# Performance work log

Measured on AMD Instinct MI355X. Metric: run time of the kernel, lower is better.

## Reference

```python
import jax, jax.numpy as jnp
import numpy as np

SQRT_DK = jnp.sqrt(jnp.float32(128.0))
BN_EPS = 1e-5


def setup_inputs() -> dict:
    key = jax.random.key(0)
    ks = jax.random.split(key, 12)
    B, C, F, Fp, K, O, DK = 4, 64, 20000, 10000, 16, 128, 128
    fea = jax.random.normal(ks[0], (B, C, F), dtype=jnp.float32)
    ring_n = jax.random.randint(ks[1], (B, Fp, K), 0, F, dtype=jnp.int64)
    pool_idx = jnp.sort(jax.random.randint(ks[2], (Fp,), 0, F, dtype=jnp.int64))
    pos_embed = jnp.zeros((1, 1, 1), dtype=jnp.float32)
    s = 1.0 / np.sqrt(C)
    Wk = jax.random.uniform(ks[3], (DK, C), jnp.float32, -s, s)
    bk = jax.random.uniform(ks[4], (DK,), jnp.float32, -s, s)
    Wq = jax.random.uniform(ks[5], (DK, C), jnp.float32, -s, s)
    bq = jax.random.uniform(ks[6], (DK,), jnp.float32, -s, s)
    Wc = jax.random.uniform(ks[7], (O, C), jnp.float32, -s, s)
    bc = jax.random.uniform(ks[8], (O,), jnp.float32, -s, s)
    gamma = jnp.ones((O,), jnp.float32)
    beta = jnp.zeros((O,), jnp.float32)
    return {"fea": fea, "ring_n": ring_n, "pool_idx": pool_idx, "pos_embed": pos_embed,
            "Wk": Wk, "bk": bk, "Wq": Wq, "bq": bq, "Wc": Wc, "bc": bc,
            "gamma": gamma, "beta": beta}


def _gather_neighbors(fea, ring_n):
    # fea: [B,C,F], ring_n: [B,Fp,K] -> [B,C,Fp,K]
    return jax.vmap(lambda f, r: f[:, r])(fea, ring_n)


def reference(fea, ring_n, pool_idx, pos_embed, Wk, bk, Wq, bq, Wc, bc, gamma, beta):
    # neighbor gather along face dim
    neighbor_fea = _gather_neighbors(fea, ring_n)            # [B,C,Fp,K]
    self_fea = fea[:, :, pool_idx][..., None]                # [B,C,Fp,1]
    cat = jnp.concatenate([self_fea, neighbor_fea], axis=3)  # [B,C,Fp,K+1]
    # per-face key (self only) and per-neighbor query (Linear4D over channel dim)
    keyv = jnp.einsum('bcfk,oc->bofk', self_fea, Wk) + bk[None, :, None, None]  # [B,128,Fp,1]
    query = jnp.einsum('bcfk,oc->bofk', cat, Wq) + bq[None, :, None, None]       # [B,128,Fp,K+1]
    att = jnp.sum(keyv * query, axis=1, keepdims=True) / SQRT_DK                 # [B,1,Fp,K+1]
    att = jax.nn.softmax(att, axis=3)
    agg = jnp.sum(cat * att, axis=3)                                             # [B,C,Fp]
    # concat_mlp: 1x1 conv + BatchNorm1d (training-mode batch stats) + ReLU
    y = jnp.einsum('bcf,oc->bof', agg, Wc) + bc[None, :, None]                   # [B,O,Fp]
    mean = jnp.mean(y, axis=(0, 2), keepdims=True)
    var = jnp.var(y, axis=(0, 2), keepdims=True)
    y = (y - mean) * jax.lax.rsqrt(var + BN_EPS)
    y = y * gamma[None, :, None] + beta[None, :, None]
    return jax.nn.relu(y)
```

## Files before the change

kernel.cpp:

```cpp
#include <hip/hip_runtime.h>

#define F_ALL 20000
#define FP    10000
#define BB    4
#define KK    16
#define OO    128
#define NFACE 40000
#define NBLK  625

#define WS_FEAT 0
#define WS_AGG  (BB*F_ALL*64)
#define WS_GP   (WS_AGG + NFACE*64)
#define WS_SAP  (WS_GP + NBLK*4096)
#define WS_MT   (WS_SAP + NBLK*64)
#define WS_V0   (WS_MT + 4096)
#define WS_G    (WS_V0 + 64)
#define WS_SUMA (WS_G + 4096)
#define WS_SC   (WS_SUMA + 64)
#define WS_SH   (WS_SC + 128)

template<int CTRL>
__device__ __forceinline__ float dpp_add(float x) {
    return x + __int_as_float(__builtin_amdgcn_update_dpp(0, __float_as_int(x), CTRL, 0xF, 0xF, true));
}
__device__ __forceinline__ float sum16(float x) {
    x = dpp_add<0x121>(x);
    x = dpp_add<0x122>(x);
    x = dpp_add<0x124>(x);
    x = dpp_add<0x128>(x);
    return x;
}

__global__ __launch_bounds__(256) void k_pre(const float* __restrict__ fea,
                                             const float* __restrict__ Wk,
                                             const float* __restrict__ bk,
                                             const float* __restrict__ Wq,
                                             float* __restrict__ ws) {
    __shared__ float tile[64][65];
    int tid = threadIdx.x;
    if (blockIdx.x < 1252) {
        int bb = blockIdx.x / 313;
        int tb = blockIdx.x % 313;
        int fbase = tb * 64;
        int x  = tid & 63;
        int y0 = tid >> 6;
        int f = fbase + x;
        float* feaT = ws + WS_FEAT;
        if (f < F_ALL) {
#pragma unroll
            for (int i = 0; i < 16; i++) {
                int c = y0 + i * 4;
                tile[c][x] = fea[((long)bb * 64 + c) * F_ALL + f];
            }
        }
        __syncthreads();
#pragma unroll
        for (int i = 0; i < 16; i++) {
            int fr = y0 + i * 4;
            int ff = fbase + fr;
            if (ff < F_ALL)
                feaT[((long)bb * F_ALL + ff) * 64 + x] = tile[x][fr];
        }
    } else {
        int idx = (blockIdx.x - 1252) * 256 + tid;
        int j = idx >> 6, i = idx & 63;
        float acc = 0.f;
#pragma unroll 8
        for (int o = 0; o < 128; o++) acc += Wq[o * 64 + i] * Wk[o * 64 + j];
        ws[WS_MT + idx] = acc;
        if (blockIdx.x == 1252 && tid < 64) {
            float a = 0.f;
            for (int o = 0; o < 128; o++) a += Wq[o * 64 + tid] * bk[o];
            ws[WS_V0 + tid] = a;
            ws[WS_SUMA + tid] = 0.f;
        }
    }
}

__global__ __launch_bounds__(256) void k_attn(const int* __restrict__ ring,
                                              const int* __restrict__ pool,
                                              float* __restrict__ ws) {
    __shared__ __align__(16) float lds[12608];
    float* At = lds;
    float* Sf = lds + 4096;
    float* U  = lds + 8256;
    int tid = threadIdx.x;
    int fbase = blockIdx.x * 64;
    const float* feaT = ws + WS_FEAT;
    const float scale = 0.08838834764831845f;

    for (int i = tid; i < 4096; i += 256) At[i] = ws[WS_MT + i];
    {
        int r = tid >> 2;
        int face = fbase + r;
        int b = face / FP;
        int p = pool[face - b * FP];
        const float* src = feaT + ((long)(b * F_ALL + p)) * 64;
        int off = (tid & 3) * 4;
#pragma unroll
        for (int it = 0; it < 4; it++, off += 16) {
            float4 v = *(const float4*)(src + off);
            Sf[r * 65 + off + 0] = v.x;
            Sf[r * 65 + off + 1] = v.y;
            Sf[r * 65 + off + 2] = v.z;
            Sf[r * 65 + off + 3] = v.w;
        }
    }
    __syncthreads();

    int ti = tid & 15, tj = tid >> 4;
    {
        int f0 = ti * 4, o0 = tj * 4;
        float4 v0 = *(const float4*)&ws[WS_V0 + o0];
        float acc[4][4];
#pragma unroll
        for (int a = 0; a < 4; a++) {
            acc[a][0] = v0.x; acc[a][1] = v0.y; acc[a][2] = v0.z; acc[a][3] = v0.w;
        }
        for (int j = 0; j < 64; j++) {
            float4 wv = *(const float4*)&At[j * 64 + o0];
#pragma unroll
            for (int a = 0; a < 4; a++) {
                float av = Sf[(f0 + a) * 65 + j];
                acc[a][0] += av * wv.x;
                acc[a][1] += av * wv.y;
                acc[a][2] += av * wv.z;
                acc[a][3] += av * wv.w;
            }
        }
#pragma unroll
        for (int a = 0; a < 4; a++)
            *(float4*)&U[(f0 + a) * 68 + o0] =
                make_float4(acc[a][0], acc[a][1], acc[a][2], acc[a][3]);
    }
    __syncthreads();

    float* Ag = At;
    int lane = tid & 63;
    int il = lane & 15, c4 = il * 4;
    for (int it = 0; it < 4; it++) {
        int fl = (tid >> 4) + it * 16;
        int face = fbase + fl;
        int b = face / FP;
        const float* fb = feaT + ((long)b * F_ALL) * 64 + c4;

        float4 sf = make_float4(Sf[fl * 65 + c4], Sf[fl * 65 + c4 + 1],
                                Sf[fl * 65 + c4 + 2], Sf[fl * 65 + c4 + 3]);
        float4 u = *(const float4*)&U[fl * 68 + c4];

        int rv = ring[face * KK + il];
        float4 nv[KK];
#pragma unroll
        for (int k = 0; k < KK; k++) {
            int rk = __shfl(rv, (lane & 48) | k, 64);
            nv[k] = *(const float4*)(fb + (long)rk * 64);
        }

        float l[KK + 1];
        l[0] = sum16(u.x * sf.x + u.y * sf.y + u.z * sf.z + u.w * sf.w) * scale;
#pragma unroll
        for (int k = 0; k < KK; k++)
            l[k + 1] = sum16(u.x * nv[k].x + u.y * nv[k].y + u.z * nv[k].z + u.w * nv[k].w) * scale;

        float m = l[0];
#pragma unroll
        for (int k = 1; k <= KK; k++) m = fmaxf(m, l[k]);
        float den = 0.f;
#pragma unroll
        for (int k = 0; k <= KK; k++) { l[k] = __expf(l[k] - m); den += l[k]; }
        float inv = 1.0f / den;

        float4 a;
        a.x = l[0] * sf.x; a.y = l[0] * sf.y; a.z = l[0] * sf.z; a.w = l[0] * sf.w;
#pragma unroll
        for (int k = 0; k < KK; k++) {
            a.x += l[k + 1] * nv[k].x;
            a.y += l[k + 1] * nv[k].y;
            a.z += l[k + 1] * nv[k].z;
            a.w += l[k + 1] * nv[k].w;
        }
        a.x *= inv; a.y *= inv; a.z *= inv; a.w *= inv;
        *(float4*)&Ag[fl * 64 + c4] = a;
        *(float4*)&ws[WS_AGG + (long)face * 64 + c4] = a;
    }
    __syncthreads();

    float acc[4][4];
#pragma unroll
    for (int a = 0; a < 4; a++)
#pragma unroll
        for (int b = 0; b < 4; b++) acc[a][b] = 0.f;
    float gacc[4] = {0.f, 0.f, 0.f, 0.f};
#pragma unroll 4
    for (int f = 0; f < 64; f++) {
        float4 av = *(const float4*)&Ag[f * 64 + ti * 4];
        float4 bv = *(const float4*)&Ag[f * 64 + tj * 4];
        float avv[4] = {av.x, av.y, av.z, av.w};
        float bvv[4] = {bv.x, bv.y, bv.z, bv.w};
#pragma unroll
        for (int a = 0; a < 4; a++) {
#pragma unroll
            for (int b = 0; b < 4; b++) acc[a][b] += avv[a] * bvv[b];
            gacc[a] += avv[a];
        }
    }
    float* gp = ws + WS_GP;
#pragma unroll
    for (int a = 0; a < 4; a++)
        *(float4*)&gp[(long)blockIdx.x * 4096 + (ti * 4 + a) * 64 + tj * 4] =
            make_float4(acc[a][0], acc[a][1], acc[a][2], acc[a][3]);
    if (tj == 0)
        *(float4*)&ws[WS_SAP + blockIdx.x * 64 + ti * 4] =
            make_float4(gacc[0], gacc[1], gacc[2], gacc[3]);
}

__global__ __launch_bounds__(256) void k_gsum(float* __restrict__ ws) {
    __shared__ float red[256];
    int t = threadIdx.x;
    if (blockIdx.x < 256) {
        const float* gp = ws + WS_GP;
        int e16 = blockIdx.x * 16;
        int e = t & 15, c = t >> 4;
        int p0 = c * 40;
        int p1 = p0 + 40; if (p1 > NBLK) p1 = NBLK;
        float s0 = 0.f, s1 = 0.f, s2 = 0.f, s3 = 0.f;
        int p = p0;
        for (; p + 4 <= p1; p += 4) {
            s0 += gp[(long)(p + 0) * 4096 + e16 + e];
            s1 += gp[(long)(p + 1) * 4096 + e16 + e];
            s2 += gp[(long)(p + 2) * 4096 + e16 + e];
            s3 += gp[(long)(p + 3) * 4096 + e16 + e];
        }
        for (; p < p1; p++) s0 += gp[(long)p * 4096 + e16 + e];
        red[t] = (s0 + s1) + (s2 + s3);
        __syncthreads();
        if (t < 16) {
            float s = 0.f;
#pragma unroll
            for (int cc = 0; cc < 16; cc++) s += red[cc * 16 + t];
            ws[WS_G + e16 + t] = s;
        }
    } else {
        const float* sap = ws + WS_SAP;
        int bq = blockIdx.x - 256;
        int e = t & 63, c = t >> 6;
        int pidx = bq * 4 + c;
        int p0 = pidx * 40;
        int p1 = p0 + 40; if (p1 > NBLK) p1 = NBLK;
        float s0 = 0.f, s1 = 0.f, s2 = 0.f, s3 = 0.f;
        int p = p0;
        for (; p + 4 <= p1; p += 4) {
            s0 += sap[(p + 0) * 64 + e];
            s1 += sap[(p + 1) * 64 + e];
            s2 += sap[(p + 2) * 64 + e];
            s3 += sap[(p + 3) * 64 + e];
        }
        for (; p < p1; p++) s0 += sap[p * 64 + e];
        red[t] = (s0 + s1) + (s2 + s3);
        __syncthreads();
        if (t < 64) {
            float tot = red[t] + red[t + 64] + red[t + 128] + red[t + 192];
            atomicAdd(&ws[WS_SUMA + t], tot);
        }
    }
}

__global__ __launch_bounds__(256) void k_stats(const float* __restrict__ Wc,
                                               const float* __restrict__ bc,
                                               const float* __restrict__ gamma,
                                               const float* __restrict__ beta,
                                               float* __restrict__ ws) {
    __shared__ float Gs[4096];
    __shared__ float gs[64];
    __shared__ float qs[256];
    int tid = threadIdx.x;
    for (int i = tid; i < 4096; i += 256) Gs[i] = ws[WS_G + i];
    if (tid < 64) gs[tid] = ws[WS_SUMA + tid];
    __syncthreads();

    int o = tid & 127, h = tid >> 7;
    float w[64];
#pragma unroll
    for (int q = 0; q < 16; q++) {
        float4 t = *(const float4*)&Wc[o * 64 + q * 4];
        w[q * 4 + 0] = t.x; w[q * 4 + 1] = t.y; w[q * 4 + 2] = t.z; w[q * 4 + 3] = t.w;
    }
    float qp = 0.f;
    for (int i = h * 32; i < h * 32 + 32; i++) {
        float t = 0.f;
#pragma unroll
        for (int j = 0; j < 64; j++) t += Gs[i * 64 + j] * w[j];
        qp += Wc[o * 64 + i] * t;
    }
    qs[tid] = qp;
    __syncthreads();
    if (h == 0) {
        const float invN = 1.0f / (float)NFACE;
        float qform = qs[o] + qs[o + 128];
        float md = 0.f;
#pragma unroll
        for (int j = 0; j < 64; j++) md += gs[j] * w[j];
        float bco = bc[o];
        float mean = md * invN + bco;
        float ey2  = (qform + 2.f * bco * md) * invN + bco * bco;
        float var  = ey2 - mean * mean;
        float sc   = gamma[o] * rsqrtf(var + 1e-5f);
        ws[WS_SC + o] = sc;
        ws[WS_SH + o] = beta[o] + (bco - mean) * sc;
    }
}

__global__ __launch_bounds__(256) void k_out(const float* __restrict__ Wc,
                                             const float* __restrict__ ws,
                                             float* __restrict__ out) {
    __shared__ __align__(16) float WcT[64 * 132];
    __shared__ __align__(16) float AgT[64 * 68];
    const float* agg = ws + WS_AGG;
    int tid = threadIdx.x;
    int fbase = blockIdx.x * 64;
    for (int i = tid; i < 128 * 64; i += 256) {
        int o = i >> 6, j = i & 63;
        WcT[j * 132 + o] = Wc[i];
    }
    for (int i = tid; i < 64 * 64; i += 256) {
        int f = i >> 6, j = i & 63;
        AgT[j * 68 + f] = agg[((long)(fbase + f)) * 64 + j];
    }
    __syncthreads();

    int tx = tid & 15, ty = tid >> 4;
    float acc[8][4];
#pragma unroll
    for (int a = 0; a < 8; a++)
#pragma unroll
        for (int b = 0; b < 4; b++) acc[a][b] = 0.f;

    for (int j = 0; j < 64; j++) {
        float4 w0 = *(const float4*)&WcT[j * 132 + ty * 8];
        float4 w1 = *(const float4*)&WcT[j * 132 + ty * 8 + 4];
        float4 a0 = *(const float4*)&AgT[j * 68 + tx * 4];
        float wv[8] = {w0.x, w0.y, w0.z, w0.w, w1.x, w1.y, w1.z, w1.w};
        float av[4] = {a0.x, a0.y, a0.z, a0.w};
#pragma unroll
        for (int oi = 0; oi < 8; oi++)
#pragma unroll
            for (int fi = 0; fi < 4; fi++) acc[oi][fi] += wv[oi] * av[fi];
    }

    int fg0 = fbase + tx * 4;
    int b   = fg0 / FP;
    int fp0 = fg0 - b * FP;
#pragma unroll
    for (int oi = 0; oi < 8; oi++) {
        int o = ty * 8 + oi;
        float sc = ws[WS_SC + o];
        float sh = ws[WS_SH + o];
        float4 v;
        v.x = fmaxf(acc[oi][0] * sc + sh, 0.f);
        v.y = fmaxf(acc[oi][1] * sc + sh, 0.f);
        v.z = fmaxf(acc[oi][2] * sc + sh, 0.f);
        v.w = fmaxf(acc[oi][3] * sc + sh, 0.f);
        *(float4*)&out[((long)(b * OO + o)) * FP + fp0] = v;
    }
}

extern "C" void kernel_launch(void* const* d_in, const int* in_sizes, int n_in,
                              void* d_out, int out_size, void* d_ws, size_t ws_size,
                              hipStream_t stream) {
    const float* fea  = (const float*)d_in[0];
    const int*   ring = (const int*)d_in[1];
    const int*   pool = (const int*)d_in[2];
    const float* Wk = (const float*)d_in[4];
    const float* bk = (const float*)d_in[5];
    const float* Wq = (const float*)d_in[6];
    const float* Wc = (const float*)d_in[8];
    const float* bc = (const float*)d_in[9];
    const float* gamma = (const float*)d_in[10];
    const float* beta  = (const float*)d_in[11];

    float* out = (float*)d_out;
    float* ws  = (float*)d_ws;

    k_pre  <<<1268, 256, 0, stream>>>(fea, Wk, bk, Wq, ws);
    k_attn <<<NBLK, 256, 0, stream>>>(ring, pool, ws);
    k_gsum <<<260,  256, 0, stream>>>(ws);
    k_stats<<<1,    256, 0, stream>>>(Wc, bc, gamma, beta, ws);
    k_out  <<<NBLK, 256, 0, stream>>>(Wc, ws, out);
}
```

Measured before the change: 173.8 us.

## Fuse all stages into one persistent cooperative kernel with grid syncs

Merges the five separate kernels into a single persistent cooperative kernel that loops over tiles and separates phases with grid-wide syncs. It falls back to four phased launches if the cooperative launch fails. Stats are now computed redundantly per block and kept in LDS instead of in a separate single-block kernel and global scratch. The aim is to remove launch gaps and the serial single-block stats launch, at the cost of grid.sync overhead, reduced occupancy (launch bounds of 2 blocks per CU, grid capped at 625), and a host occupancy query on every call.

Measured after the change: 300.8 us. 73.1% more time.

```diff
diff --git a/kernel.cpp b/kernel.cpp
--- a/kernel.cpp
+++ b/kernel.cpp
@@ -1,4 +1,7 @@
 #include <hip/hip_runtime.h>
+#include <hip/hip_cooperative_groups.h>
+
+namespace cg = cooperative_groups;
 
 #define F_ALL 20000
 #define FP    10000
@@ -6,18 +9,22 @@
 #define KK    16
 #define OO    128
 #define NFACE 40000
-#define NBLK  625
+#define NTILE 625
 
 #define WS_FEAT 0
 #define WS_AGG  (BB*F_ALL*64)
 #define WS_GP   (WS_AGG + NFACE*64)
-#define WS_SAP  (WS_GP + NBLK*4096)
-#define WS_MT   (WS_SAP + NBLK*64)
+#define WS_SAP  (WS_GP + NTILE*4096)
+#define WS_MT   (WS_SAP + NTILE*64)
 #define WS_V0   (WS_MT + 4096)
 #define WS_G    (WS_V0 + 64)
 #define WS_SUMA (WS_G + 4096)
-#define WS_SC   (WS_SUMA + 64)
-#define WS_SH   (WS_SC + 128)
+
+#define L_R1   4352
+#define L_GS   8448
+#define L_QS   8512
+#define L_SC   12800
+#define L_SH   12928
 
 template<int CTRL>
 __device__ __forceinline__ float dpp_add(float x) {
@@ -31,336 +38,363 @@
     return x;
 }
 
-__global__ __launch_bounds__(256) void k_pre(const float* __restrict__ fea,
-                                             const float* __restrict__ Wk,
-                                             const float* __restrict__ bk,
-                                             const float* __restrict__ Wq,
-                                             float* __restrict__ ws) {
-    __shared__ float tile[64][65];
-    int tid = threadIdx.x;
-    if (blockIdx.x < 1252) {
-        int bb = blockIdx.x / 313;
-        int tb = blockIdx.x % 313;
-        int fbase = tb * 64;
-        int x  = tid & 63;
-        int y0 = tid >> 6;
-        int f = fbase + x;
+__global__ __launch_bounds__(256, 2) void k_fused(const float* __restrict__ fea,
+                                                  const int* __restrict__ ring,
+                                                  const int* __restrict__ pool,
+                                                  const float* __restrict__ Wk,
+                                                  const float* __restrict__ bk,
+                                                  const float* __restrict__ Wq,
+                                                  const float* __restrict__ Wc,
+                                                  const float* __restrict__ bc,
+                                                  const float* __restrict__ gamma,
+                                                  const float* __restrict__ beta,
+                                                  float* __restrict__ ws,
+                                                  float* __restrict__ out,
+                                                  int phase) {
+    __shared__ __align__(16) float lds[13056];
+    cg::grid_group grid = cg::this_grid();
+    const int tid  = threadIdx.x;
+    const int bid  = blockIdx.x;
+    const int GRID = gridDim.x;
+    const bool coop = (phase < 0);
+    const float scale = 0.08838834764831845f;
+
+    if (coop || phase == 0) {
+        float* tile = lds;
         float* feaT = ws + WS_FEAT;
-        if (f < F_ALL) {
+        for (int tb = bid; tb < 1252; tb += GRID) {
+            __syncthreads();
+            int bb = tb / 313;
+            int fbase = (tb % 313) * 64;
+            int x  = tid & 63;
+            int y0 = tid >> 6;
+            int f = fbase + x;
+            if (f < F_ALL) {
+#pragma unroll
+                for (int i = 0; i < 16; i++) {
+                    int c = y0 + i * 4;
+                    tile[c * 65 + x] = fea[((long)bb * 64 + c) * F_ALL + f];
+                }
+            }
+            __syncthreads();
 #pragma unroll
             for (int i = 0; i < 16; i++) {
-                int c = y0 + i * 4;
-                tile[c][x] = fea[((long)bb * 64 + c) * F_ALL + f];
-            }
-        }
-        __syncthreads();
-#pragma unroll
-        for (int i = 0; i < 16; i++) {
-            int fr = y0 + i * 4;
-            int ff = fbase + fr;
-            if (ff < F_ALL)
-                feaT[((long)bb * F_ALL + ff) * 64 + x] = tile[x][fr];
-        }
-    } else {
-        int idx = (blockIdx.x - 1252) * 256 + tid;
-        int j = idx >> 6, i = idx & 63;
-        float acc = 0.f;
+                int fr = y0 + i * 4;
+                int ff = fbase + fr;
+                if (ff < F_ALL)
+                    feaT[((long)bb * F_ALL + ff) * 64 + x] = tile[x * 65 + fr];
+            }
+        }
+        if (bid < 16) {
+            int idx = bid * 256 + tid;
+            int j = idx >> 6, i = idx & 63;
+            float acc = 0.f;
 #pragma unroll 8
-        for (int o = 0; o < 128; o++) acc += Wq[o * 64 + i] * Wk[o * 64 + j];
-        ws[WS_MT + idx] = acc;
-        if (blockIdx.x == 1252 && tid < 64) {
+            for (int o = 0; o < 128; o++) acc += Wq[o * 64 + i] * Wk[o * 64 + j];
+            ws[WS_MT + idx] = acc;
+        } else if (bid == 16 && tid < 64) {
             float a = 0.f;
             for (int o = 0; o < 128; o++) a += Wq[o * 64 + tid] * bk[o];
             ws[WS_V0 + tid] = a;
             ws[WS_SUMA + tid] = 0.f;
         }
     }
-}
-
-__global__ __launch_bounds__(256) void k_attn(const int* __restrict__ ring,
-                                              const int* __restrict__ pool,
-                                              float* __restrict__ ws) {
-    __shared__ __align__(16) float lds[12608];
-    float* At = lds;
-    float* Sf = lds + 4096;
-    float* U  = lds + 8256;
-    int tid = threadIdx.x;
-    int fbase = blockIdx.x * 64;
-    const float* feaT = ws + WS_FEAT;
-    const float scale = 0.08838834764831845f;
-
-    for (int i = tid; i < 4096; i += 256) At[i] = ws[WS_MT + i];
-    {
-        int r = tid >> 2;
-        int face = fbase + r;
-        int b = face / FP;
-        int p = pool[face - b * FP];
-        const float* src = feaT + ((long)(b * F_ALL + p)) * 64;
-        int off = (tid & 3) * 4;
-#pragma unroll
-        for (int it = 0; it < 4; it++, off += 16) {
-            float4 v = *(const float4*)(src + off);
-            Sf[r * 65 + off + 0] = v.x;
-            Sf[r * 65 + off + 1] = v.y;
-            Sf[r * 65 + off + 2] = v.z;
-            Sf[r * 65 + off + 3] = v.w;
-        }
-    }
-    __syncthreads();
-
-    int ti = tid & 15, tj = tid >> 4;
-    {
-        int f0 = ti * 4, o0 = tj * 4;
-        float4 v0 = *(const float4*)&ws[WS_V0 + o0];
-        float acc[4][4];
-#pragma unroll
-        for (int a = 0; a < 4; a++) {
-            acc[a][0] = v0.x; acc[a][1] = v0.y; acc[a][2] = v0.z; acc[a][3] = v0.w;
-        }
-        for (int j = 0; j < 64; j++) {
-            float4 wv = *(const float4*)&At[j * 64 + o0];
-#pragma unroll
-            for (int a = 0; a < 4; a++) {
-                float av = Sf[(f0 + a) * 65 + j];
-                acc[a][0] += av * wv.x;
-                acc[a][1] += av * wv.y;
-                acc[a][2] += av * wv.z;
-                acc[a][3] += av * wv.w;
-            }
-        }
-#pragma unroll
-        for (int a = 0; a < 4; a++)
-            *(float4*)&U[(f0 + a) * 68 + o0] =
-                make_float4(acc[a][0], acc[a][1], acc[a][2], acc[a][3]);
-    }
-    __syncthreads();
-
-    float* Ag = At;
-    int lane = tid & 63;
-    int il = lane & 15, c4 = il * 4;
-    for (int it = 0; it < 4; it++) {
-        int fl = (tid >> 4) + it * 16;
-        int face = fbase + fl;
-        int b = face / FP;
-        const float* fb = feaT + ((long)b * F_ALL) * 64 + c4;
-
-        float4 sf = make_float4(Sf[fl * 65 + c4], Sf[fl * 65 + c4 + 1],
-                                Sf[fl * 65 + c4 + 2], Sf[fl * 65 + c4 + 3]);
-        float4 u = *(const float4*)&U[fl * 68 + c4];
-
-        int rv = ring[face * KK + il];
-        float4 nv[KK];
-#pragma unroll
-        for (int k = 0; k < KK; k++) {
-            int rk = __shfl(rv, (lane & 48) | k, 64);
-            nv[k] = *(const float4*)(fb + (long)rk * 64);
-        }
-
-        float l[KK + 1];
-        l[0] = sum16(u.x * sf.x + u.y * sf.y + u.z * sf.z + u.w * sf.w) * scale;
-#pragma unroll
-        for (int k = 0; k < KK; k++)
-            l[k + 1] = sum16(u.x * nv[k].x + u.y * nv[k].y + u.z * nv[k].z + u.w * nv[k].w) * scale;
-
-        float m = l[0];
-#pragma unroll
-        for (int k = 1; k <= KK; k++) m = fmaxf(m, l[k]);
-        float den = 0.f;
-#pragma unroll
-        for (int k = 0; k <= KK; k++) { l[k] = __expf(l[k] - m); den += l[k]; }
-        float inv = 1.0f / den;
-
-        float4 a;
-        a.x = l[0] * sf.x; a.y = l[0] * sf.y; a.z = l[0] * sf.z; a.w = l[0] * sf.w;
-#pragma unroll
-        for (int k = 0; k < KK; k++) {
-            a.x += l[k + 1] * nv[k].x;
-            a.y += l[k + 1] * nv[k].y;
-            a.z += l[k + 1] * nv[k].z;
-            a.w += l[k + 1] * nv[k].w;
-        }
-        a.x *= inv; a.y *= inv; a.z *= inv; a.w *= inv;
-        *(float4*)&Ag[fl * 64 + c4] = a;
-        *(float4*)&ws[WS_AGG + (long)face * 64 + c4] = a;
-    }
-    __syncthreads();
-
-    float acc[4][4];
-#pragma unroll
-    for (int a = 0; a < 4; a++)
-#pragma unroll
-        for (int b = 0; b < 4; b++) acc[a][b] = 0.f;
-    float gacc[4] = {0.f, 0.f, 0.f, 0.f};
+    if (coop) grid.sync();
+
+    if (coop || phase == 1) {
+        float* Sf = lds;
+        float* U  = lds + L_R1;
+        float* At = lds + 8704;
+        const float* feaT = ws + WS_FEAT;
+        int ti = tid & 15, tj = tid >> 4;
+        int lane = tid & 63;
+        int il = lane & 15, c4 = il * 4;
+
+        for (int i = tid; i < 4096; i += 256) At[i] = ws[WS_MT + i];
+
+        for (int tile = bid; tile < NTILE; tile += GRID) {
+            int fbase = tile * 64;
+            __syncthreads();
+
+            {
+                int r = tid >> 2;
+                int face = fbase + r;
+                int b = face / FP;
+                int p = pool[face - b * FP];
+                const float* src = feaT + ((long)(b * F_ALL + p)) * 64;
+                int off = (tid & 3) * 4;
+#pragma unroll
+                for (int it = 0; it < 4; it++, off += 16) {
+                    float4 v = *(const float4*)(src + off);
+                    Sf[r * 65 + off + 0] = v.x;
+                    Sf[r * 65 + off + 1] = v.y;
+                    Sf[r * 65 + off + 2] = v.z;
+                    Sf[r * 65 + off + 3] = v.w;
+                }
+            }
+            __syncthreads();
+
+            {
+                int f0 = ti * 4, o0 = tj * 4;
+                float4 v0 = *(const float4*)&ws[WS_V0 + o0];
+                float acc[4][4];
+#pragma unroll
+                for (int a = 0; a < 4; a++) {
+                    acc[a][0] = v0.x; acc[a][1] = v0.y; acc[a][2] = v0.z; acc[a][3] = v0.w;
+                }
+                for (int j = 0; j < 64; j++) {
+                    float4 wv = *(const float4*)&At[j * 64 + o0];
+#pragma unroll
+                    for (int a = 0; a < 4; a++) {
+                        float av = Sf[(f0 + a) * 65 + j];
+                        acc[a][0] += av * wv.x;
+                        acc[a][1] += av * wv.y;
+                        acc[a][2] += av * wv.z;
+                        acc[a][3] += av * wv.w;
+                    }
+                }
+#pragma unroll
+                for (int a = 0; a < 4; a++)
+                    *(float4*)&U[(f0 + a) * 68 + o0] =
+                        make_float4(acc[a][0], acc[a][1], acc[a][2], acc[a][3]);
+            }
+            __syncthreads();
+
+            float4 a_res[4];
+            for (int it = 0; it < 4; it++) {
+                int fl = (tid >> 4) + it * 16;
+                int face = fbase + fl;
+                int b = face / FP;
+                const float* fb = feaT + ((long)b * F_ALL) * 64 + c4;
+
+                float4 sf = make_float4(Sf[fl * 65 + c4], Sf[fl * 65 + c4 + 1],
+                                        Sf[fl * 65 + c4 + 2], Sf[fl * 65 + c4 + 3]);
+                float4 u = *(const float4*)&U[fl * 68 + c4];
+
+                int rv = ring[face * KK + il];
+                float4 nv[KK];
+#pragma unroll
+                for (int k = 0; k < KK; k++) {
+                    int rk = __shfl(rv, (lane & 48) | k, 64);
+                    nv[k] = *(const float4*)(fb + (long)rk * 64);
+                }
+
+                float l[KK + 1];
+                l[0] = sum16(u.x * sf.x + u.y * sf.y + u.z * sf.z + u.w * sf.w) * scale;
+#pragma unroll
+                for (int k = 0; k < KK; k++)
+                    l[k + 1] = sum16(u.x * nv[k].x + u.y * nv[k].y + u.z * nv[k].z + u.w * nv[k].w) * scale;
+
+                float m = l[0];
+#pragma unroll
+                for (int k = 1; k <= KK; k++) m = fmaxf(m, l[k]);
+                float den = 0.f;
+#pragma unroll
+                for (int k = 0; k <= KK; k++) { l[k] = __expf(l[k] - m); den += l[k]; }
+                float inv = 1.0f / den;
+
+                float4 a;
+                a.x = l[0] * sf.x; a.y = l[0] * sf.y; a.z = l[0] * sf.z; a.w = l[0] * sf.w;
+#pragma unroll
+                for (int k = 0; k < KK; k++) {
+                    a.x += l[k + 1] * nv[k].x;
+                    a.y += l[k + 1] * nv[k].y;
+                    a.z += l[k + 1] * nv[k].z;
+                    a.w += l[k + 1] * nv[k].w;
+                }
+                a.x *= inv; a.y *= inv; a.z *= inv; a.w *= inv;
+                a_res[it] = a;
+                *(float4*)&ws[WS_AGG + (long)face * 64 + c4] = a;
+            }
+            __syncthreads();
+            float* Ag = lds;
+#pragma unroll
+            for (int it = 0; it < 4; it++) {
+                int fl = (tid >> 4) + it * 16;
+                *(float4*)&Ag[fl * 64 + c4] = a_res[it];
+            }
+            __syncthreads();
+
+            float acc[4][4];
+#pragma unroll
+            for (int a = 0; a < 4; a++)
+#pragma unroll
+                for (int b = 0; b < 4; b++) acc[a][b] = 0.f;
+            float gacc[4] = {0.f, 0.f, 0.f, 0.f};
 #pragma unroll 4
-    for (int f = 0; f < 64; f++) {
-        float4 av = *(const float4*)&Ag[f * 64 + ti * 4];
-        float4 bv = *(const float4*)&Ag[f * 64 + tj * 4];
-        float avv[4] = {av.x, av.y, av.z, av.w};
-        float bvv[4] = {bv.x, bv.y, bv.z, bv.w};
-#pragma unroll
-        for (int a = 0; a < 4; a++) {
-#pragma unroll
-            for (int b = 0; b < 4; b++) acc[a][b] += avv[a] * bvv[b];
-            gacc[a] += avv[a];
-        }
-    }
-    float* gp = ws + WS_GP;
-#pragma unroll
-    for (int a = 0; a < 4; a++)
-        *(float4*)&gp[(long)blockIdx.x * 4096 + (ti * 4 + a) * 64 + tj * 4] =
-            make_float4(acc[a][0], acc[a][1], acc[a][2], acc[a][3]);
-    if (tj == 0)
-        *(float4*)&ws[WS_SAP + blockIdx.x * 64 + ti * 4] =
-            make_float4(gacc[0], gacc[1], gacc[2], gacc[3]);
-}
-
-__global__ __launch_bounds__(256) void k_gsum(float* __restrict__ ws) {
-    __shared__ float red[256];
-    int t = threadIdx.x;
-    if (blockIdx.x < 256) {
-        const float* gp = ws + WS_GP;
-        int e16 = blockIdx.x * 16;
-        int e = t & 15, c = t >> 4;
-        int p0 = c * 40;
-        int p1 = p0 + 40; if (p1 > NBLK) p1 = NBLK;
-        float s0 = 0.f, s1 = 0.f, s2 = 0.f, s3 = 0.f;
-        int p = p0;
-        for (; p + 4 <= p1; p += 4) {
-            s0 += gp[(long)(p + 0) * 4096 + e16 + e];
-            s1 += gp[(long)(p + 1) * 4096 + e16 + e];
-            s2 += gp[(long)(p + 2) * 4096 + e16 + e];
-            s3 += gp[(long)(p + 3) * 4096 + e16 + e];
-        }
-        for (; p < p1; p++) s0 += gp[(long)p * 4096 + e16 + e];
-        red[t] = (s0 + s1) + (s2 + s3);
-        __syncthreads();
-        if (t < 16) {
-            float s = 0.f;
-#pragma unroll
-            for (int cc = 0; cc < 16; cc++) s += red[cc * 16 + t];
-            ws[WS_G + e16 + t] = s;
-        }
-    } else {
-        const float* sap = ws + WS_SAP;
-        int bq = blockIdx.x - 256;
-        int e = t & 63, c = t >> 6;
-        int pidx = bq * 4 + c;
-        int p0 = pidx * 40;
-        int p1 = p0 + 40; if (p1 > NBLK) p1 = NBLK;
-        float s0 = 0.f, s1 = 0.f, s2 = 0.f, s3 = 0.f;
-        int p = p0;
-        for (; p + 4 <= p1; p += 4) {
-            s0 += sap[(p + 0) * 64 + e];
-            s1 += sap[(p + 1) * 64 + e];
-            s2 += sap[(p + 2) * 64 + e];
-            s3 += sap[(p + 3) * 64 + e];
-        }
-        for (; p < p1; p++) s0 += sap[p * 64 + e];
-        red[t] = (s0 + s1) + (s2 + s3);
-        __syncthreads();
-        if (t < 64) {
-            float tot = red[t] + red[t + 64] + red[t + 128] + red[t + 192];
-            atomicAdd(&ws[WS_SUMA + t], tot);
-        }
-    }
-}
-
-__global__ __launch_bounds__(256) void k_stats(const float* __restrict__ Wc,
-                                               const float* __restrict__ bc,
-                                               const float* __restrict__ gamma,
-                                               const float* __restrict__ beta,
-                                               float* __restrict__ ws) {
-    __shared__ float Gs[4096];
-    __shared__ float gs[64];
-    __shared__ float qs[256];
-    int tid = threadIdx.x;
-    for (int i = tid; i < 4096; i += 256) Gs[i] = ws[WS_G + i];
-    if (tid < 64) gs[tid] = ws[WS_SUMA + tid];
-    __syncthreads();
-
-    int o = tid & 127, h = tid >> 7;
-    float w[64];
-#pragma unroll
-    for (int q = 0; q < 16; q++) {
-        float4 t = *(const float4*)&Wc[o * 64 + q * 4];
-        w[q * 4 + 0] = t.x; w[q * 4 + 1] = t.y; w[q * 4 + 2] = t.z; w[q * 4 + 3] = t.w;
-    }
-    float qp = 0.f;
-    for (int i = h * 32; i < h * 32 + 32; i++) {
-        float t = 0.f;
-#pragma unroll
-        for (int j = 0; j < 64; j++) t += Gs[i * 64 + j] * w[j];
-        qp += Wc[o * 64 + i] * t;
-    }
-    qs[tid] = qp;
-    __syncthreads();
-    if (h == 0) {
-        const float invN = 1.0f / (float)NFACE;
-        float qform = qs[o] + qs[o + 128];
-        float md = 0.f;
-#pragma unroll
-        for (int j = 0; j < 64; j++) md += gs[j] * w[j];
-        float bco = bc[o];
-        float mean = md * invN + bco;
-        float ey2  = (qform + 2.f * bco * md) * invN + bco * bco;
-        float var  = ey2 - mean * mean;
-        float sc   = gamma[o] * rsqrtf(var + 1e-5f);
-        ws[WS_SC + o] = sc;
-        ws[WS_SH + o] = beta[o] + (bco - mean) * sc;
-    }
-}
-
-__global__ __launch_bounds__(256) void k_out(const float* __restrict__ Wc,
-                                             const float* __restrict__ ws,
-                                             float* __restrict__ out) {
-    __shared__ __align__(16) float WcT[64 * 132];
-    __shared__ __align__(16) float AgT[64 * 68];
-    const float* agg = ws + WS_AGG;
-    int tid = threadIdx.x;
-    int fbase = blockIdx.x * 64;
-    for (int i = tid; i < 128 * 64; i += 256) {
-        int o = i >> 6, j = i & 63;
-        WcT[j * 132 + o] = Wc[i];
-    }
-    for (int i = tid; i < 64 * 64; i += 256) {
-        int f = i >> 6, j = i & 63;
-        AgT[j * 68 + f] = agg[((long)(fbase + f)) * 64 + j];
-    }
-    __syncthreads();
-
-    int tx = tid & 15, ty = tid >> 4;
-    float acc[8][4];
-#pragma unroll
-    for (int a = 0; a < 8; a++)
-#pragma unroll
-        for (int b = 0; b < 4; b++) acc[a][b] = 0.f;
-
-    for (int j = 0; j < 64; j++) {
-        float4 w0 = *(const float4*)&WcT[j * 132 + ty * 8];
-        float4 w1 = *(const float4*)&WcT[j * 132 + ty * 8 + 4];
-        float4 a0 = *(const float4*)&AgT[j * 68 + tx * 4];
-        float wv[8] = {w0.x, w0.y, w0.z, w0.w, w1.x, w1.y, w1.z, w1.w};
-        float av[4] = {a0.x, a0.y, a0.z, a0.w};
-#pragma unroll
-        for (int oi = 0; oi < 8; oi++)
-#pragma unroll
-            for (int fi = 0; fi < 4; fi++) acc[oi][fi] += wv[oi] * av[fi];
-    }
-
-    int fg0 = fbase + tx * 4;
-    int b   = fg0 / FP;
-    int fp0 = fg0 - b * FP;
-#pragma unroll
-    for (int oi = 0; oi < 8; oi++) {
-        int o = ty * 8 + oi;
-        float sc = ws[WS_SC + o];
-        float sh = ws[WS_SH + o];
-        float4 v;
-        v.x = fmaxf(acc[oi][0] * sc + sh, 0.f);
-        v.y = fmaxf(acc[oi][1] * sc + sh, 0.f);
-        v.z = fmaxf(acc[oi][2] * sc + sh, 0.f);
-        v.w = fmaxf(acc[oi][3] * sc + sh, 0.f);
-        *(float4*)&out[((long)(b * OO + o)) * FP + fp0] = v;
+            for (int f = 0; f < 64; f++) {
+                float4 av = *(const float4*)&Ag[f * 64 + ti * 4];
+                float4 bv = *(const float4*)&Ag[f * 64 + tj * 4];
+                float avv[4] = {av.x, av.y, av.z, av.w};
+                float bvv[4] = {bv.x, bv.y, bv.z, bv.w};
+#pragma unroll
+                for (int a = 0; a < 4; a++) {
+#pragma unroll
+                    for (int b = 0; b < 4; b++) acc[a][b] += avv[a] * bvv[b];
+                    gacc[a] += avv[a];
+                }
+            }
+            float* gp = ws + WS_GP;
+#pragma unroll
+            for (int a = 0; a < 4; a++)
+                *(float4*)&gp[(long)tile * 4096 + (ti * 4 + a) * 64 + tj * 4] =
+                    make_float4(acc[a][0], acc[a][1], acc[a][2], acc[a][3]);
+            if (tj == 0)
+                *(float4*)&ws[WS_SAP + tile * 64 + ti * 4] =
+                    make_float4(gacc[0], gacc[1], gacc[2], gacc[3]);
+        }
+    }
+    if (coop) grid.sync();
+
+    if (coop || phase == 2) {
+        float* red = lds;
+        for (int v = bid; v < 260; v += GRID) {
+            __syncthreads();
+            if (v < 256) {
+                const float* gp = ws + WS_GP;
+                int e16 = v * 16;
+                int e = tid & 15, c = tid >> 4;
+                int p0 = c * 40;
+                int p1 = p0 + 40; if (p1 > NTILE) p1 = NTILE;
+                float s0 = 0.f, s1 = 0.f, s2 = 0.f, s3 = 0.f;
+                int p = p0;
+                for (; p + 4 <= p1; p += 4) {
+                    s0 += gp[(long)(p + 0) * 4096 + e16 + e];
+                    s1 += gp[(long)(p + 1) * 4096 + e16 + e];
+                    s2 += gp[(long)(p + 2) * 4096 + e16 + e];
+                    s3 += gp[(long)(p + 3) * 4096 + e16 + e];
+                }
+                for (; p < p1; p++) s0 += gp[(long)p * 4096 + e16 + e];
+                red[tid] = (s0 + s1) + (s2 + s3);
+                __syncthreads();
+                if (tid < 16) {
+                    float s = 0.f;
+#pragma unroll
+                    for (int cc = 0; cc < 16; cc++) s += red[cc * 16 + tid];
+                    ws[WS_G + e16 + tid] = s;
+                }
+            } else {
+                const float* sap = ws + WS_SAP;
+                int bq = v - 256;
+                int e = tid & 63, c = tid >> 6;
+                int pidx = bq * 4 + c;
+                int p0 = pidx * 40;
+                int p1 = p0 + 40; if (p1 > NTILE) p1 = NTILE;
+                float s0 = 0.f, s1 = 0.f, s2 = 0.f, s3 = 0.f;
+                int p = p0;
+                for (; p + 4 <= p1; p += 4) {
+                    s0 += sap[(p + 0) * 64 + e];
+                    s1 += sap[(p + 1) * 64 + e];
+                    s2 += sap[(p + 2) * 64 + e];
+                    s3 += sap[(p + 3) * 64 + e];
+                }
+                for (; p < p1; p++) s0 += sap[p * 64 + e];
+                red[tid] = (s0 + s1) + (s2 + s3);
+                __syncthreads();
+                if (tid < 64) {
+                    float tot = red[tid] + red[tid + 64] + red[tid + 128] + red[tid + 192];
+                    atomicAdd(&ws[WS_SUMA + tid], tot);
+                }
+            }
+        }
+    }
+    if (coop) grid.sync();
+
+    if (coop || phase == 3) {
+        {
+            float* Gs = lds + L_R1;
+            float* gs = lds + L_GS;
+            float* qs = lds + L_QS;
+            __syncthreads();
+            for (int i = tid; i < 4096; i += 256) Gs[i] = ws[WS_G + i];
+            if (tid < 64) gs[tid] = ws[WS_SUMA + tid];
+            __syncthreads();
+
+            int o = tid & 127, h = tid >> 7;
+            float w[64];
+#pragma unroll
+            for (int q = 0; q < 16; q++) {
+                float4 t = *(const float4*)&Wc[o * 64 + q * 4];
+                w[q * 4 + 0] = t.x; w[q * 4 + 1] = t.y; w[q * 4 + 2] = t.z; w[q * 4 + 3] = t.w;
+            }
+            float qp = 0.f;
+            for (int i = h * 32; i < h * 32 + 32; i++) {
+                float t = 0.f;
+#pragma unroll
+                for (int j = 0; j < 64; j++) t += Gs[i * 64 + j] * w[j];
+                qp += Wc[o * 64 + i] * t;
+            }
+            qs[tid] = qp;
+            __syncthreads();
+            if (h == 0) {
+                const float invN = 1.0f / (float)NFACE;
+                float qform = qs[o] + qs[o + 128];
+                float md = 0.f;
+#pragma unroll
+                for (int j = 0; j < 64; j++) md += gs[j] * w[j];
+                float bco = bc[o];
+                float mean = md * invN + bco;
+                float ey2  = (qform + 2.f * bco * md) * invN + bco * bco;
+                float var  = ey2 - mean * mean;
+                float sc   = gamma[o] * rsqrtf(var + 1e-5f);
+                lds[L_SC + o] = sc;
+                lds[L_SH + o] = beta[o] + (bco - mean) * sc;
+            }
+            __syncthreads();
+        }
+        {
+            float* AgT = lds;
+            float* WcT = lds + L_R1;
+            const float* agg = ws + WS_AGG;
+            for (int i = tid; i < 128 * 64; i += 256) {
+                int o = i >> 6, j = i & 63;
+                WcT[j * 132 + o] = Wc[i];
+            }
+            int tx = tid & 15, ty = tid >> 4;
+            for (int tile = bid; tile < NTILE; tile += GRID) {
+                int fbase = tile * 64;
+                __syncthreads();
+                for (int i = tid; i < 64 * 64; i += 256) {
+                    int f = i >> 6, j = i & 63;
+                    AgT[j * 68 + f] = agg[((long)(fbase + f)) * 64 + j];
+                }
+                __syncthreads();
+
+                float acc[8][4];
+#pragma unroll
+                for (int a = 0; a < 8; a++)
+#pragma unroll
+                    for (int b = 0; b < 4; b++) acc[a][b] = 0.f;
+
+                for (int j = 0; j < 64; j++) {
+                    float4 w0 = *(const float4*)&WcT[j * 132 + ty * 8];
+                    float4 w1 = *(const float4*)&WcT[j * 132 + ty * 8 + 4];
+                    float4 a0 = *(const float4*)&AgT[j * 68 + tx * 4];
+                    float wv[8] = {w0.x, w0.y, w0.z, w0.w, w1.x, w1.y, w1.z, w1.w};
+                    float av[4] = {a0.x, a0.y, a0.z, a0.w};
+#pragma unroll
+                    for (int oi = 0; oi < 8; oi++)
+#pragma unroll
+                        for (int fi = 0; fi < 4; fi++) acc[oi][fi] += wv[oi] * av[fi];
+                }
+
+                int fg0 = fbase + tx * 4;
+                int b   = fg0 / FP;
+                int fp0 = fg0 - b * FP;
+#pragma unroll
+                for (int oi = 0; oi < 8; oi++) {
+                    int o = ty * 8 + oi;
+                    float sc = lds[L_SC + o];
+                    float sh = lds[L_SH + o];
+                    float4 v;
+                    v.x = fmaxf(acc[oi][0] * sc + sh, 0.f);
+                    v.y = fmaxf(acc[oi][1] * sc + sh, 0.f);
+                    v.z = fmaxf(acc[oi][2] * sc + sh, 0.f);
+                    v.w = fmaxf(acc[oi][3] * sc + sh, 0.f);
+                    *(float4*)&out[((long)(b * OO + o)) * FP + fp0] = v;
+                }
+            }
+        }
     }
 }
 
@@ -381,9 +415,22 @@
     float* out = (float*)d_out;
     float* ws  = (float*)d_ws;
 
-    k_pre  <<<1268, 256, 0, stream>>>(fea, Wk, bk, Wq, ws);
-    k_attn <<<NBLK, 256, 0, stream>>>(ring, pool, ws);
-    k_gsum <<<260,  256, 0, stream>>>(ws);
-    k_stats<<<1,    256, 0, stream>>>(Wc, bc, gamma, beta, ws);
-    k_out  <<<NBLK, 256, 0, stream>>>(Wc, ws, out);
+    int maxb = 0;
+    hipError_t qe = hipOccupancyMaxActiveBlocksPerMultiprocessor(&maxb, (const void*)k_fused, 256, 0);
+    int grid = (qe == hipSuccess && maxb > 0) ? maxb * 256 : 0;
+    if (grid > NTILE) grid = NTILE;
+
+    hipError_t le = hipErrorUnknown;
+    if (grid >= 64) {
+        int phase = -1;
+        void* kargs[] = {(void*)&fea, (void*)&ring, (void*)&pool, (void*)&Wk, (void*)&bk,
+                         (void*)&Wq, (void*)&Wc, (void*)&bc, (void*)&gamma, (void*)&beta,
+                         (void*)&ws, (void*)&out, (void*)&phase};
+        le = hipLaunchCooperativeKernel((const void*)k_fused, dim3(grid), dim3(256), kargs, 0, stream);
+    }
+    if (le != hipSuccess) {
+        for (int ph = 0; ph < 4; ph++)
+            k_fused<<<512, 256, 0, stream>>>(fea, ring, pool, Wk, bk, Wq, Wc, bc,
+                                             gamma, beta, ws, out, ph);
+    }
 }
```

## Split Gram accumulation into separate kernel and shrink attention blocks to 32 faces

Applied to the files above, without the earlier changes.

The attention kernel now handles 32 faces per block instead of 64. It computes each face's query-key projection inline per lane group rather than as a separate block GEMM stage with extra barriers, and drops the U and aggregated-tile LDS buffers. This cuts shared memory per block to raise occupancy for the latency-bound neighbor gather. The Gram and column-sum accumulation moves to a new k_gram kernel that rereads the aggregated features from global memory over 320 faces per block. That yields fewer partials to reduce, at the cost of an extra launch and an extra pass over the aggregate buffer.

Result: slower. 181.6 us (+4.5%).

```diff
diff --git a/kernel.cpp b/kernel.cpp
--- a/kernel.cpp
+++ b/kernel.cpp
@@ -6,13 +6,13 @@
 #define KK    16
 #define OO    128
 #define NFACE 40000
-#define NBLK  625
+#define NGRAMB 125
 
 #define WS_FEAT 0
 #define WS_AGG  (BB*F_ALL*64)
 #define WS_GP   (WS_AGG + NFACE*64)
-#define WS_SAP  (WS_GP + NBLK*4096)
-#define WS_MT   (WS_SAP + NBLK*64)
+#define WS_SAP  (WS_GP + NGRAMB*4096)
+#define WS_MT   (WS_SAP + NGRAMB*64)
 #define WS_V0   (WS_MT + 4096)
 #define WS_G    (WS_V0 + 64)
 #define WS_SUMA (WS_G + 4096)
@@ -80,65 +80,33 @@
 __global__ __launch_bounds__(256) void k_attn(const int* __restrict__ ring,
                                               const int* __restrict__ pool,
                                               float* __restrict__ ws) {
-    __shared__ __align__(16) float lds[12608];
-    float* At = lds;
-    float* Sf = lds + 4096;
-    float* U  = lds + 8256;
-    int tid = threadIdx.x;
-    int fbase = blockIdx.x * 64;
+    __shared__ __align__(16) float MTl[4096];
+    __shared__ float Sf[32 * 65];
+    int tid = threadIdx.x;
+    int fbase = blockIdx.x * 32;
     const float* feaT = ws + WS_FEAT;
     const float scale = 0.08838834764831845f;
 
-    for (int i = tid; i < 4096; i += 256) At[i] = ws[WS_MT + i];
+    for (int i = tid; i < 4096; i += 256) MTl[i] = ws[WS_MT + i];
     {
-        int r = tid >> 2;
+        int r = tid >> 3;
         int face = fbase + r;
         int b = face / FP;
         int p = pool[face - b * FP];
-        const float* src = feaT + ((long)(b * F_ALL + p)) * 64;
-        int off = (tid & 3) * 4;
-#pragma unroll
-        for (int it = 0; it < 4; it++, off += 16) {
-            float4 v = *(const float4*)(src + off);
-            Sf[r * 65 + off + 0] = v.x;
-            Sf[r * 65 + off + 1] = v.y;
-            Sf[r * 65 + off + 2] = v.z;
-            Sf[r * 65 + off + 3] = v.w;
-        }
+        const float* src = feaT + ((long)(b * F_ALL + p)) * 64 + (tid & 7) * 8;
+        float4 v0 = *(const float4*)src;
+        float4 v1 = *(const float4*)(src + 4);
+        float* dst = &Sf[r * 65 + (tid & 7) * 8];
+        dst[0] = v0.x; dst[1] = v0.y; dst[2] = v0.z; dst[3] = v0.w;
+        dst[4] = v1.x; dst[5] = v1.y; dst[6] = v1.z; dst[7] = v1.w;
     }
     __syncthreads();
 
-    int ti = tid & 15, tj = tid >> 4;
-    {
-        int f0 = ti * 4, o0 = tj * 4;
-        float4 v0 = *(const float4*)&ws[WS_V0 + o0];
-        float acc[4][4];
-#pragma unroll
-        for (int a = 0; a < 4; a++) {
-            acc[a][0] = v0.x; acc[a][1] = v0.y; acc[a][2] = v0.z; acc[a][3] = v0.w;
-        }
-        for (int j = 0; j < 64; j++) {
-            float4 wv = *(const float4*)&At[j * 64 + o0];
-#pragma unroll
-            for (int a = 0; a < 4; a++) {
-                float av = Sf[(f0 + a) * 65 + j];
-                acc[a][0] += av * wv.x;
-                acc[a][1] += av * wv.y;
-                acc[a][2] += av * wv.z;
-                acc[a][3] += av * wv.w;
-            }
-        }
-#pragma unroll
-        for (int a = 0; a < 4; a++)
-            *(float4*)&U[(f0 + a) * 68 + o0] =
-                make_float4(acc[a][0], acc[a][1], acc[a][2], acc[a][3]);
-    }
-    __syncthreads();
-
-    float* Ag = At;
     int lane = tid & 63;
     int il = lane & 15, c4 = il * 4;
-    for (int it = 0; it < 4; it++) {
+    float4 uv0 = *(const float4*)&ws[WS_V0 + c4];
+
+    for (int it = 0; it < 2; it++) {
         int fl = (tid >> 4) + it * 16;
         int face = fbase + fl;
         int b = face / FP;
@@ -146,7 +114,6 @@
 
         float4 sf = make_float4(Sf[fl * 65 + c4], Sf[fl * 65 + c4 + 1],
                                 Sf[fl * 65 + c4 + 2], Sf[fl * 65 + c4 + 3]);
-        float4 u = *(const float4*)&U[fl * 68 + c4];
 
         int rv = ring[face * KK + il];
         float4 nv[KK];
@@ -154,6 +121,17 @@
         for (int k = 0; k < KK; k++) {
             int rk = __shfl(rv, (lane & 48) | k, 64);
             nv[k] = *(const float4*)(fb + (long)rk * 64);
+        }
+
+        float4 u = uv0;
+#pragma unroll 8
+        for (int j = 0; j < 64; j++) {
+            float aj = Sf[fl * 65 + j];
+            float4 m4 = *(const float4*)&MTl[j * 64 + c4];
+            u.x += m4.x * aj;
+            u.y += m4.y * aj;
+            u.z += m4.z * aj;
+            u.w += m4.w * aj;
         }
 
         float l[KK + 1];
@@ -180,28 +158,41 @@
             a.w += l[k + 1] * nv[k].w;
         }
         a.x *= inv; a.y *= inv; a.z *= inv; a.w *= inv;
-        *(float4*)&Ag[fl * 64 + c4] = a;
         *(float4*)&ws[WS_AGG + (long)face * 64 + c4] = a;
     }
-    __syncthreads();
-
+}
+
+__global__ __launch_bounds__(256) void k_gram(float* __restrict__ ws) {
+    __shared__ float lbuf[4096];
+    const float* agg = ws + WS_AGG;
+    int tid = threadIdx.x;
+    int ti = tid & 15, tj = tid >> 4;
     float acc[4][4];
 #pragma unroll
     for (int a = 0; a < 4; a++)
 #pragma unroll
         for (int b = 0; b < 4; b++) acc[a][b] = 0.f;
     float gacc[4] = {0.f, 0.f, 0.f, 0.f};
+
+    for (int c = 0; c < 5; c++) {
+        int fbase = blockIdx.x * 320 + c * 64;
+        const float4* src = (const float4*)(agg + (long)fbase * 64);
+        float4* dst = (float4*)lbuf;
+        __syncthreads();
+        for (int i = tid; i < 1024; i += 256) dst[i] = src[i];
+        __syncthreads();
 #pragma unroll 4
-    for (int f = 0; f < 64; f++) {
-        float4 av = *(const float4*)&Ag[f * 64 + ti * 4];
-        float4 bv = *(const float4*)&Ag[f * 64 + tj * 4];
-        float avv[4] = {av.x, av.y, av.z, av.w};
-        float bvv[4] = {bv.x, bv.y, bv.z, bv.w};
-#pragma unroll
-        for (int a = 0; a < 4; a++) {
-#pragma unroll
-            for (int b = 0; b < 4; b++) acc[a][b] += avv[a] * bvv[b];
-            gacc[a] += avv[a];
+        for (int f = 0; f < 64; f++) {
+            float4 av = *(const float4*)&lbuf[f * 64 + ti * 4];
+            float4 bv = *(const float4*)&lbuf[f * 64 + tj * 4];
+            float avv[4] = {av.x, av.y, av.z, av.w};
+            float bvv[4] = {bv.x, bv.y, bv.z, bv.w};
+#pragma unroll
+            for (int a = 0; a < 4; a++) {
+#pragma unroll
+                for (int b = 0; b < 4; b++) acc[a][b] += avv[a] * bvv[b];
+                gacc[a] += avv[a];
+            }
         }
     }
     float* gp = ws + WS_GP;
@@ -221,8 +212,8 @@
         const float* gp = ws + WS_GP;
         int e16 = blockIdx.x * 16;
         int e = t & 15, c = t >> 4;
-        int p0 = c * 40;
-        int p1 = p0 + 40; if (p1 > NBLK) p1 = NBLK;
+        int p0 = c * 8;
+        int p1 = p0 + 8; if (p1 > NGRAMB) p1 = NGRAMB;
         float s0 = 0.f, s1 = 0.f, s2 = 0.f, s3 = 0.f;
         int p = p0;
         for (; p + 4 <= p1; p += 4) {
@@ -245,8 +236,8 @@
         int bq = blockIdx.x - 256;
         int e = t & 63, c = t >> 6;
         int pidx = bq * 4 + c;
-        int p0 = pidx * 40;
-        int p1 = p0 + 40; if (p1 > NBLK) p1 = NBLK;
+        int p0 = pidx * 8;
+        int p1 = p0 + 8; if (p1 > NGRAMB) p1 = NGRAMB;
         float s0 = 0.f, s1 = 0.f, s2 = 0.f, s3 = 0.f;
         int p = p0;
         for (; p + 4 <= p1; p += 4) {
@@ -382,8 +373,9 @@
     float* ws  = (float*)d_ws;
 
     k_pre  <<<1268, 256, 0, stream>>>(fea, Wk, bk, Wq, ws);
-    k_attn <<<NBLK, 256, 0, stream>>>(ring, pool, ws);
+    k_attn <<<1250, 256, 0, stream>>>(ring, pool, ws);
+    k_gram <<<NGRAMB, 256, 0, stream>>>(ws);
     k_gsum <<<260,  256, 0, stream>>>(ws);
     k_stats<<<1,    256, 0, stream>>>(Wc, bc, gamma, beta, ws);
-    k_out  <<<NBLK, 256, 0, stream>>>(Wc, ws, out);
-}
+    k_out  <<<625,  256, 0, stream>>>(Wc, ws, out);
+}
```
